# Kernel optimization log

Measured on AMD Instinct MI355X. Metric: run time of the kernel, lower is better.

Reference implementation:

```python
import jax, jax.numpy as jnp
import numpy as np
from jax import lax

EPS = 1e-5
GROUPS = 8
NUM_HEADS = 8


def setup_inputs() -> dict:
    key = jax.random.key(0)
    ks = jax.random.split(key, 3)
    C = 512
    x = jax.random.normal(ks[0], (8, C, 32, 32), dtype=jnp.float32)
    gamma = jnp.ones((C,), jnp.float32)
    beta = jnp.zeros((C,), jnp.float32)
    w_qkv = jax.random.normal(ks[1], (3 * C, C), dtype=jnp.float32) * (1.0 / np.sqrt(C))
    b_qkv = jnp.zeros((3 * C,), jnp.float32)
    w_proj = jax.random.normal(ks[2], (C, C), dtype=jnp.float32) * (1.0 / np.sqrt(C))
    b_proj = jnp.zeros((C,), jnp.float32)
    return {"x": x, "gamma": gamma, "beta": beta, "w_qkv": w_qkv,
            "b_qkv": b_qkv, "w_proj": w_proj, "b_proj": b_proj}


def reference(x, gamma, beta, w_qkv, b_qkv, w_proj, b_proj):
    b, c, h, w = x.shape
    hd = c // NUM_HEADS
    L = h * w
    # GroupNorm over (c/G, h, w) per group
    xg = x.reshape(b, GROUPS, c // GROUPS, h, w)
    mean = jnp.mean(xg, axis=(2, 3, 4), keepdims=True)
    var = jnp.var(xg, axis=(2, 3, 4), keepdims=True)
    xn = ((xg - mean) * lax.rsqrt(var + EPS)).reshape(b, c, h, w)
    xn = xn * gamma[None, :, None, None] + beta[None, :, None, None]
    # 1x1 conv QKV projection over flattened spatial dim
    xr = xn.reshape(b, c, L)
    qkv = jnp.einsum('oc,bcl->bol', w_qkv, xr) + b_qkv[None, :, None]
    q, k, v = jnp.split(qkv, 3, axis=1)
    # [b, H, L, hd]
    q = q.reshape(b, NUM_HEADS, hd, L).transpose(0, 1, 3, 2)
    k = k.reshape(b, NUM_HEADS, hd, L).transpose(0, 1, 3, 2)
    v = v.reshape(b, NUM_HEADS, hd, L).transpose(0, 1, 3, 2)
    scale = 1.0 / np.sqrt(hd).astype(np.float32)
    attn = jnp.einsum('bhqd,bhkd->bhqk', q, k) * scale
    attn = jax.nn.softmax(attn, axis=-1)
    out = jnp.einsum('bhqk,bhkd->bhqd', attn, v)  # [b, H, L, hd]
    out = out.transpose(0, 1, 3, 2).reshape(b, c, L)
    out = jnp.einsum('oc,bcl->bol', w_proj, out) + b_proj[None, :, None]
    return x + out.reshape(b, c, h, w)
```

## Files before the change

kernel.cpp:

```cpp
#include <hip/hip_runtime.h>
#include <hip/hip_bf16.h>

typedef unsigned short u16;
typedef __attribute__((ext_vector_type(8))) short short8;
typedef __attribute__((ext_vector_type(4))) float floatx4;
typedef __attribute__((ext_vector_type(16))) float floatx16;
typedef __attribute__((ext_vector_type(4))) unsigned uint4v;

struct __attribute__((aligned(8))) u16x4 { u16 x, y, z, w; };
struct __attribute__((aligned(16))) u16x8 { u16 v[8]; };

__device__ __forceinline__ u16 f2bf(float f) {
  unsigned u = __builtin_bit_cast(unsigned, f);
  u += 0x7fff + ((u >> 16) & 1);
  return (u16)(u >> 16);
}

__device__ __forceinline__ unsigned cvt_pk_bf16(float lo, float hi) {
  unsigned d;
  asm("v_cvt_pk_bf16_f32 %0, %1, %2" : "=v"(d) : "v"(lo), "v"(hi));
  return d;
}

__device__ __forceinline__ void gload_lds16(const u16* g, u16* l) {
  __builtin_amdgcn_global_load_lds(
      (const __attribute__((address_space(1))) void*)g,
      (__attribute__((address_space(3))) void*)l, 16, 0, 0);
}

__global__ __launch_bounds__(256) void k_convert(
    const float* __restrict__ wq, const float* __restrict__ wp,
    u16* __restrict__ oq, u16* __restrict__ op) {
  int t = blockIdx.x * 256 + threadIdx.x;
  constexpr int NQ4 = (1536 * 512) / 4;
  constexpr int NP4 = (512 * 512) / 4;
  if (t < NQ4) {
    float4 v = reinterpret_cast<const float4*>(wq)[t];
    u16x4 o = { f2bf(v.x), f2bf(v.y), f2bf(v.z), f2bf(v.w) };
    reinterpret_cast<u16x4*>(oq)[t] = o;
  } else if (t - NQ4 < NP4) {
    int i = t - NQ4;
    float4 v = reinterpret_cast<const float4*>(wp)[i];
    u16x4 o = { f2bf(v.x), f2bf(v.y), f2bf(v.z), f2bf(v.w) };
    reinterpret_cast<u16x4*>(op)[i] = o;
  }
}

__global__ __launch_bounds__(256) void k_gn_stats(const float* __restrict__ x,
                                                  float* __restrict__ stats) {
  int bg = blockIdx.x >> 3, sl = blockIdx.x & 7;
  int b = bg >> 3, g = bg & 7;
  const float* base = x + ((size_t)(b * 512 + g * 64) * 1024) + sl * 128;
  float s = 0.f, ss = 0.f;
#pragma unroll
  for (int i = 0; i < 8; ++i) {
    int idx = threadIdx.x + i * 256;
    int c = idx >> 5, l4 = idx & 31;
    float4 v = *reinterpret_cast<const float4*>(base + (size_t)c * 1024 + l4 * 4);
    s += v.x + v.y + v.z + v.w;
    ss += v.x * v.x + v.y * v.y + v.z * v.z + v.w * v.w;
  }
#pragma unroll
  for (int d = 1; d < 64; d <<= 1) { s += __shfl_xor(s, d); ss += __shfl_xor(ss, d); }
  __shared__ float rs[4], rss[4];
  int wid = threadIdx.x >> 6;
  if ((threadIdx.x & 63) == 0) { rs[wid] = s; rss[wid] = ss; }
  __syncthreads();
  if (threadIdx.x == 0) {
    stats[(bg * 8 + sl) * 2]     = rs[0] + rs[1] + rs[2] + rs[3];
    stats[(bg * 8 + sl) * 2 + 1] = rss[0] + rss[1] + rss[2] + rss[3];
  }
}

__global__ __launch_bounds__(256) void k_gn_norm(
    const float* __restrict__ x, const float* __restrict__ gamma,
    const float* __restrict__ beta, const float* __restrict__ stats,
    u16* __restrict__ xnT) {
  int bg = blockIdx.x >> 3, sl = blockIdx.x & 7;
  int b = bg >> 3, g = bg & 7;
  float s = 0.f, ss = 0.f;
#pragma unroll
  for (int i = 0; i < 8; ++i) { s += stats[(bg * 8 + i) * 2]; ss += stats[(bg * 8 + i) * 2 + 1]; }
  const float inv_n = 1.0f / 65536.0f;
  float mean = s * inv_n;
  float var = ss * inv_n - mean * mean;
  float istd = rsqrtf(var + 1e-5f);
  __shared__ float tile[128 * 65];
  const float* base = x + ((size_t)(b * 512 + g * 64) * 1024) + sl * 128;
#pragma unroll
  for (int i = 0; i < 8; ++i) {
    int idx = threadIdx.x + i * 256;
    int c = idx >> 5, l4 = idx & 31;
    float4 v = *reinterpret_cast<const float4*>(base + (size_t)c * 1024 + l4 * 4);
    float gm = gamma[g * 64 + c];
    float ga = gm * istd;
    float be = beta[g * 64 + c] - mean * ga;
    tile[(l4 * 4 + 0) * 65 + c] = v.x * ga + be;
    tile[(l4 * 4 + 1) * 65 + c] = v.y * ga + be;
    tile[(l4 * 4 + 2) * 65 + c] = v.z * ga + be;
    tile[(l4 * 4 + 3) * 65 + c] = v.w * ga + be;
  }
  __syncthreads();
  u16* obase = xnT + ((size_t)(b * 1024 + sl * 128) * 512) + g * 64;
#pragma unroll
  for (int i = 0; i < 8; ++i) {
    int idx = threadIdx.x + i * 256;
    int l = idx >> 4, c4 = (idx & 15) * 4;
    u16x4 o = { f2bf(tile[l * 65 + c4]),     f2bf(tile[l * 65 + c4 + 1]),
                f2bf(tile[l * 65 + c4 + 2]), f2bf(tile[l * 65 + c4 + 3]) };
    *reinterpret_cast<u16x4*>(obase + (size_t)l * 512 + c4) = o;
  }
}

template <int MODE>
__global__ __launch_bounds__(256) void k_gemm(
    const u16* __restrict__ A, const u16* __restrict__ Bm,
    const float* __restrict__ bias, const float* __restrict__ xres,
    u16* __restrict__ Qb, u16* __restrict__ Kb, u16* __restrict__ Vb,
    float* __restrict__ out) {
  int b = blockIdx.x & 7;
  int rem = blockIdx.x >> 3;
  int mt = rem >> 3, nt = rem & 7;
  int tid = threadIdx.x;
  int lane = tid & 63, wid = tid >> 6;
  int wm = wid >> 1, wn = wid & 1;

  union SM {
    u16 ab[2][2][128 * 64];
    u16 c16[128 * 136];
    float c32[128 * 128];
  };
  __shared__ SM sm;

  floatx4 z = {0.f, 0.f, 0.f, 0.f};
  floatx4 acc[4][4];
#pragma unroll
  for (int m = 0; m < 4; ++m)
#pragma unroll
    for (int n = 0; n < 4; ++n) acc[m][n] = z;

  const u16* Abase = A + (size_t)(mt * 128) * 512;
  const u16* Bbase = Bm + ((size_t)(b * 1024 + nt * 128)) * 512;
  int cb0 = (lane & 7) ^ (lane >> 3);
  const u16* asrc = Abase + (size_t)(wid * 32 + (lane >> 3)) * 512 + cb0 * 8;
  const u16* bsrc = Bbase + (size_t)(wid * 32 + (lane >> 3)) * 512 + cb0 * 8;

#define STAGE(BUF, KK)                                                           \
  {                                                                              \
    _Pragma("unroll")                                                            \
    for (int j = 0; j < 4; ++j) {                                                \
      gload_lds16(asrc + (size_t)j * 8 * 512 + (KK) * 64,                        \
                  &sm.ab[BUF][0][wid * 2048 + j * 512]);                         \
      gload_lds16(bsrc + (size_t)j * 8 * 512 + (KK) * 64,                        \
                  &sm.ab[BUF][1][wid * 2048 + j * 512]);                         \
    }                                                                            \
  }

  STAGE(0, 0);
#pragma unroll
  for (int kk = 0; kk < 8; ++kk) {
    const int cur = kk & 1;
    if (kk < 7) {
      STAGE(cur ^ 1, kk + 1);
      asm volatile("s_waitcnt vmcnt(8)" ::: "memory");
    } else {
      asm volatile("s_waitcnt vmcnt(0)" ::: "memory");
    }
    __builtin_amdgcn_s_barrier();
    __builtin_amdgcn_sched_barrier(0);
    const u16* Asc = sm.ab[cur][0];
    const u16* Bsc = sm.ab[cur][1];
#pragma unroll
    for (int kc = 0; kc < 2; ++kc) {
      int cbk = kc * 4 + (lane >> 4);
      short8 af[4], bf[4];
#pragma unroll
      for (int m = 0; m < 4; ++m) {
        int row = wm * 64 + m * 16 + (lane & 15);
        af[m] = *reinterpret_cast<const short8*>(Asc + row * 64 + ((cbk ^ (row & 7)) * 8));
      }
#pragma unroll
      for (int n = 0; n < 4; ++n) {
        int row = wn * 64 + n * 16 + (lane & 15);
        bf[n] = *reinterpret_cast<const short8*>(Bsc + row * 64 + ((cbk ^ (row & 7)) * 8));
      }
#pragma unroll
      for (int m = 0; m < 4; ++m)
#pragma unroll
        for (int n = 0; n < 4; ++n)
          acc[m][n] = __builtin_amdgcn_mfma_f32_16x16x32_bf16(af[m], bf[n], acc[m][n], 0, 0, 0);
    }
    __builtin_amdgcn_s_barrier();
  }
#undef STAGE

  int sec = (MODE == 0) ? (mt >> 2) : 0;
  int ow0 = (mt & 3) * 128;
#pragma unroll
  for (int m = 0; m < 4; ++m) {
#pragma unroll
    for (int n = 0; n < 4; ++n) {
#pragma unroll
      for (int r = 0; r < 4; ++r) {
        int o_l = wm * 64 + m * 16 + ((lane >> 4) * 4) + r;
        int l_l = wn * 64 + n * 16 + (lane & 15);
        float v = acc[m][n][r] + bias[mt * 128 + o_l];
        if (MODE == 0) {
          if (sec == 0) v *= 0.18033688f;
          u16 bv = f2bf(v);
          if (sec < 2) sm.c16[l_l * 136 + o_l] = bv;
          else         sm.c16[o_l * 136 + l_l] = bv;
        } else {
          sm.c32[o_l * 128 + l_l] = v;
        }
      }
    }
  }
  __syncthreads();
  if (MODE == 0) {
    u16* dst = (sec == 0) ? Qb : (sec == 1 ? Kb : Vb);
#pragma unroll
    for (int p = 0; p < 8; ++p) {
      int row = p * 16 + (tid >> 4);
      int col = (tid & 15) * 8;
      u16x8 vv = *reinterpret_cast<const u16x8*>(&sm.c16[row * 136 + col]);
      size_t gi;
      if (sec < 2) gi = ((size_t)(b * 1024 + nt * 128 + row)) * 512 + ow0 + col;
      else         gi = ((size_t)(b * 512 + ow0 + row)) * 1024 + nt * 128 + col;
      *reinterpret_cast<u16x8*>(dst + gi) = vv;
    }
  } else {
#pragma unroll
    for (int p = 0; p < 16; ++p) {
      int row = p * 8 + (tid >> 5);
      int col = (tid & 31) * 4;
      float4 vv = *reinterpret_cast<const float4*>(&sm.c32[row * 128 + col]);
      size_t gi = ((size_t)(b * 512 + mt * 128 + row)) * 1024 + nt * 128 + col;
      float4 xr = *reinterpret_cast<const float4*>(xres + gi);
      vv.x += xr.x; vv.y += xr.y; vv.z += xr.z; vv.w += xr.w;
      *reinterpret_cast<float4*>(out + gi) = vv;
    }
  }
}

__global__ __launch_bounds__(256) void k_attn(
    const u16* __restrict__ Qb, const u16* __restrict__ Kb,
    const u16* __restrict__ Vb, u16* __restrict__ OT) {
  int b = blockIdx.x & 7;
  int h = (blockIdx.x >> 3) & 7;
  int qt = blockIdx.x >> 6;
  int tid = threadIdx.x;
  int lane = tid & 63, wid = tid >> 6;
  int l31 = lane & 31, g = lane >> 5;
  int r7 = l31 & 7;
  __shared__ u16 Ks[64 * 64], Vs[64 * 64];

  short8 qf[4];
  int qrow = qt * 128 + wid * 32 + l31;
  const u16* qp = Qb + ((size_t)(b * 1024 + qrow)) * 512 + h * 64 + g * 8;
#pragma unroll
  for (int kc2 = 0; kc2 < 4; ++kc2)
    qf[kc2] = *reinterpret_cast<const short8*>(qp + kc2 * 16);

  floatx16 oacc[2];
#pragma unroll
  for (int nd = 0; nd < 2; ++nd)
#pragma unroll
    for (int r = 0; r < 16; ++r) oacc[nd][r] = 0.f;
  float m = -1e30f, se = 0.f;

  const u16* ksrc[2]; const u16* vsrc[2]; int sdst[2];
#pragma unroll
  for (int i = 0; i < 2; ++i) {
    int idx = tid + i * 256;
    int row = idx >> 3, cb = idx & 7;
    ksrc[i] = Kb + ((size_t)(b * 1024 + row)) * 512 + h * 64 + cb * 8;
    vsrc[i] = Vb + ((size_t)(b * 512 + h * 64 + row)) * 1024 + cb * 8;
    sdst[i] = row * 64 + ((cb ^ (row & 7)) * 8);
  }
  short8 kreg[2], vreg[2];
#pragma unroll
  for (int i = 0; i < 2; ++i) {
    kreg[i] = *reinterpret_cast<const short8*>(ksrc[i]);
    vreg[i] = *reinterpret_cast<const short8*>(vsrc[i]);
  }

  for (int kt = 0; kt < 16; ++kt) {
#pragma unroll
    for (int i = 0; i < 2; ++i) {
      *reinterpret_cast<short8*>(Ks + sdst[i]) = kreg[i];
      *reinterpret_cast<short8*>(Vs + sdst[i]) = vreg[i];
    }
    __syncthreads();
    if (kt < 15) {
#pragma unroll
      for (int i = 0; i < 2; ++i) {
        kreg[i] = *reinterpret_cast<const short8*>(ksrc[i] + (size_t)(kt + 1) * 64 * 512);
        vreg[i] = *reinterpret_cast<const short8*>(vsrc[i] + (kt + 1) * 64);
      }
    }
    floatx16 sacc[2];
#pragma unroll
    for (int nk = 0; nk < 2; ++nk)
#pragma unroll
      for (int r = 0; r < 16; ++r) sacc[nk][r] = 0.f;
#pragma unroll
    for (int nk = 0; nk < 2; ++nk) {
      const u16* krow = Ks + (nk * 32 + l31) * 64;
#pragma unroll
      for (int kc2 = 0; kc2 < 4; ++kc2) {
        int cb = kc2 * 2 + g;
        short8 kf = *reinterpret_cast<const short8*>(krow + ((cb ^ r7) * 8));
        sacc[nk] = __builtin_amdgcn_mfma_f32_32x32x16_bf16(kf, qf[kc2], sacc[nk], 0, 0, 0);
      }
    }
    float pmax = sacc[0][0];
#pragma unroll
    for (int r = 1; r < 16; ++r) pmax = fmaxf(pmax, sacc[0][r]);
#pragma unroll
    for (int r = 0; r < 16; ++r) pmax = fmaxf(pmax, sacc[1][r]);
    pmax = fmaxf(pmax, __shfl_xor(pmax, 32));
    if (__any(pmax > m + 8.0f)) {
      float mn = fmaxf(m, pmax);
      float f = __builtin_amdgcn_exp2f(m - mn);
      m = mn;
      se *= f;
#pragma unroll
      for (int nd = 0; nd < 2; ++nd)
#pragma unroll
        for (int r = 0; r < 16; ++r) oacc[nd][r] *= f;
    }
    float sum = 0.f;
#pragma unroll
    for (int nk = 0; nk < 2; ++nk)
#pragma unroll
      for (int r = 0; r < 16; ++r) {
        float pv = __builtin_amdgcn_exp2f(sacc[nk][r] - m);
        sacc[nk][r] = pv;
        sum += pv;
      }
    sum += __shfl_xor(sum, 32);
    se += sum;
#pragma unroll
    for (int nk = 0; nk < 2; ++nk) {
#pragma unroll
      for (int kc = 0; kc < 2; ++kc) {
        int base = kc * 8;
        unsigned w0 = cvt_pk_bf16(sacc[nk][base + 0], sacc[nk][base + 1]);
        unsigned w2 = cvt_pk_bf16(sacc[nk][base + 4], sacc[nk][base + 5]);
        auto s0 = __builtin_amdgcn_permlane32_swap((int)w0, (int)w2, false, false);
        unsigned w1 = cvt_pk_bf16(sacc[nk][base + 2], sacc[nk][base + 3]);
        unsigned w3 = cvt_pk_bf16(sacc[nk][base + 6], sacc[nk][base + 7]);
        auto s1 = __builtin_amdgcn_permlane32_swap((int)w1, (int)w3, false, false);
        short8 pf = __builtin_bit_cast(short8,
            uint4v{(unsigned)s0[0], (unsigned)s1[0], (unsigned)s0[1], (unsigned)s1[1]});
#pragma unroll
        for (int nd = 0; nd < 2; ++nd) {
          const u16* vrow = Vs + (nd * 32 + l31) * 64;
          int cb = nk * 4 + kc * 2 + g;
          short8 vf = *reinterpret_cast<const short8*>(vrow + ((cb ^ r7) * 8));
          oacc[nd] = __builtin_amdgcn_mfma_f32_32x32x16_bf16(vf, pf, oacc[nd], 0, 0, 0);
        }
      }
    }
    __syncthreads();
  }
  float inv = 1.0f / se;
  u16* obase = OT + ((size_t)(b * 1024 + qrow)) * 512 + h * 64;
#pragma unroll
  for (int nd = 0; nd < 2; ++nd) {
#pragma unroll
    for (int rq = 0; rq < 4; ++rq) {
      u16x4 o = { f2bf(oacc[nd][rq * 4 + 0] * inv), f2bf(oacc[nd][rq * 4 + 1] * inv),
                  f2bf(oacc[nd][rq * 4 + 2] * inv), f2bf(oacc[nd][rq * 4 + 3] * inv) };
      *reinterpret_cast<u16x4*>(obase + nd * 32 + rq * 8 + g * 4) = o;
    }
  }
}

extern "C" void kernel_launch(void* const* d_in, const int* in_sizes, int n_in,
                              void* d_out, int out_size, void* d_ws, size_t ws_size,
                              hipStream_t stream) {
  const float* x      = (const float*)d_in[0];
  const float* gamma  = (const float*)d_in[1];
  const float* beta   = (const float*)d_in[2];
  const float* w_qkv  = (const float*)d_in[3];
  const float* b_qkv  = (const float*)d_in[4];
  const float* w_proj = (const float*)d_in[5];
  const float* b_proj = (const float*)d_in[6];
  float* out = (float*)d_out;

  char* ws = (char*)d_ws;
  size_t off = 0;
  float* stats = (float*)(ws + off); off += 4096;
  u16* wqb = (u16*)(ws + off); off += (size_t)1536 * 512 * 2;
  u16* wpb = (u16*)(ws + off); off += (size_t)512 * 512 * 2;
  u16* xnT = (u16*)(ws + off); off += (size_t)8 * 1024 * 512 * 2;
  u16* Qb  = (u16*)(ws + off); off += (size_t)8 * 1024 * 512 * 2;
  u16* Kb  = (u16*)(ws + off); off += (size_t)8 * 1024 * 512 * 2;
  u16* Vb  = (u16*)(ws + off); off += (size_t)8 * 1024 * 512 * 2;
  u16* OT  = (u16*)(ws + off); off += (size_t)8 * 1024 * 512 * 2;
  if (ws_size < off) return;

  k_convert<<<1024, 256, 0, stream>>>(w_qkv, w_proj, wqb, wpb);
  k_gn_stats<<<512, 256, 0, stream>>>(x, stats);
  k_gn_norm<<<512, 256, 0, stream>>>(x, gamma, beta, stats, xnT);
  k_gemm<0><<<768, 256, 0, stream>>>(wqb, xnT, b_qkv, nullptr, Qb, Kb, Vb, nullptr);
  k_attn<<<512, 256, 0, stream>>>(Qb, Kb, Vb, OT);
  k_gemm<1><<<256, 256, 0, stream>>>(wpb, OT, b_proj, x, nullptr, nullptr, nullptr, out);
}
```

Measured before the change: 85.98 us.

## Split QKV GEMM into 256x256-tile 8-wave kernel with staged quadrant pipeline

Replaces the templated 128x128 GEMM for the QKV projection with a dedicated kernel that uses 256x256 tiles, 512 threads, and a four-phase schedule. Each phase loads one half of A or B for the next k-step while computing one quadrant of MFMAs. The epilogue is split into two halves so the staging buffer fits in shared memory. Both GEMMs also raise wave priority around their MFMA blocks. Larger tiles increase operand reuse, but with only 192 blocks on 256 CUs part of the GPU sits idle, and the extra barriers add synchronization cost.

```diff
diff --git a/kernel.cpp b/kernel.cpp
--- a/kernel.cpp
+++ b/kernel.cpp
@@ -112,11 +112,188 @@
   }
 }
 
-template <int MODE>
-__global__ __launch_bounds__(256) void k_gemm(
+__global__ __launch_bounds__(512) void k_qkv(
+    const u16* __restrict__ A, const u16* __restrict__ Bm,
+    const float* __restrict__ bias,
+    u16* __restrict__ Qb, u16* __restrict__ Kb, u16* __restrict__ Vb) {
+  int b = blockIdx.x & 7;
+  int rem = blockIdx.x >> 3;
+  int mt = rem >> 2, nt = rem & 3;
+  int tid = threadIdx.x;
+  int lane = tid & 63, wid = tid >> 6;
+  int wm = wid >> 2, wn = wid & 3;
+  int l15 = lane & 15, l4 = lane >> 4;
+
+  union SM {
+    u16 ab[2][2][256 * 64];
+    u16 cqk[256 * 136];
+    u16 cv[128 * 264];
+  };
+  __shared__ SM sm;
+
+  floatx4 acc[8][4];
+#pragma unroll
+  for (int m = 0; m < 8; ++m)
+#pragma unroll
+    for (int n = 0; n < 4; ++n) acc[m][n] = floatx4{0.f, 0.f, 0.f, 0.f};
+
+  const u16* Ab = A + (size_t)(mt * 256) * 512;
+  const u16* Bb = Bm + ((size_t)(b * 1024 + nt * 256)) * 512;
+  int cb0 = (lane & 7) ^ (lane >> 3);
+  const u16* asrc = Ab + (size_t)(wid * 16 + (lane >> 3)) * 512 + cb0 * 8;
+  const u16* bsrc = Bb + (size_t)(wid * 16 + (lane >> 3)) * 512 + cb0 * 8;
+
+  auto STG = [&](int ab, int bufn, int h, int kt) {
+    const u16* s = (ab ? bsrc : asrc) + (size_t)h * 128 * 512 + kt * 64;
+    u16* d = &sm.ab[ab][bufn][(h * 128 + wid * 16) * 64];
+    gload_lds16(s, d);
+    gload_lds16(s + 8 * 512, d + 8 * 64);
+  };
+  auto rd = [&](const u16* base, int rowbase, int kc) -> short8 {
+    int row = rowbase + l15;
+    int cbk = kc * 4 + l4;
+    return *reinterpret_cast<const short8*>(base + row * 64 + ((cbk ^ (row & 7)) * 8));
+  };
+
+  STG(0, 0, 0, 0); STG(1, 0, 0, 0); STG(0, 0, 1, 0); STG(1, 0, 1, 0);
+
+#pragma unroll
+  for (int t = 0; t < 8; ++t) {
+    const int buf = t & 1, nbuf = buf ^ 1;
+    const int kt1 = (t < 7) ? (t + 1) : 7;
+    const u16* Ac = sm.ab[0][buf];
+    const u16* Bc = sm.ab[1][buf];
+    short8 af0[4][2], af1[4][2], bflo[2][2], bfhi[2][2];
+
+    STG(0, nbuf, 0, kt1);
+    asm volatile("s_waitcnt vmcnt(4)" ::: "memory");
+    __builtin_amdgcn_s_barrier();
+    __builtin_amdgcn_sched_barrier(0);
+#pragma unroll
+    for (int m = 0; m < 4; ++m) {
+      af0[m][0] = rd(Ac, m * 32 + wm * 16, 0);
+      af0[m][1] = rd(Ac, m * 32 + wm * 16, 1);
+    }
+#pragma unroll
+    for (int n = 0; n < 2; ++n) {
+      bflo[n][0] = rd(Bc, n * 64 + wn * 16, 0);
+      bflo[n][1] = rd(Bc, n * 64 + wn * 16, 1);
+    }
+    __builtin_amdgcn_s_setprio(1);
+#pragma unroll
+    for (int kc = 0; kc < 2; ++kc)
+#pragma unroll
+      for (int m = 0; m < 4; ++m)
+#pragma unroll
+        for (int n = 0; n < 2; ++n)
+          acc[m][n] = __builtin_amdgcn_mfma_f32_16x16x32_bf16(af0[m][kc], bflo[n][kc], acc[m][n], 0, 0, 0);
+    __builtin_amdgcn_s_setprio(0);
+    __builtin_amdgcn_s_barrier();
+
+    STG(1, nbuf, 0, kt1);
+    asm volatile("s_waitcnt vmcnt(4)" ::: "memory");
+    __builtin_amdgcn_s_barrier();
+    __builtin_amdgcn_sched_barrier(0);
+#pragma unroll
+    for (int m = 0; m < 4; ++m) {
+      af1[m][0] = rd(Ac, 128 + m * 32 + wm * 16, 0);
+      af1[m][1] = rd(Ac, 128 + m * 32 + wm * 16, 1);
+    }
+    __builtin_amdgcn_s_setprio(1);
+#pragma unroll
+    for (int kc = 0; kc < 2; ++kc)
+#pragma unroll
+      for (int m = 0; m < 4; ++m)
+#pragma unroll
+        for (int n = 0; n < 2; ++n)
+          acc[4 + m][n] = __builtin_amdgcn_mfma_f32_16x16x32_bf16(af1[m][kc], bflo[n][kc], acc[4 + m][n], 0, 0, 0);
+    __builtin_amdgcn_s_setprio(0);
+    __builtin_amdgcn_s_barrier();
+
+    STG(0, nbuf, 1, kt1);
+    __builtin_amdgcn_s_barrier();
+#pragma unroll
+    for (int n = 0; n < 2; ++n) {
+      bfhi[n][0] = rd(Bc, 128 + n * 64 + wn * 16, 0);
+      bfhi[n][1] = rd(Bc, 128 + n * 64 + wn * 16, 1);
+    }
+    __builtin_amdgcn_s_setprio(1);
+#pragma unroll
+    for (int kc = 0; kc < 2; ++kc)
+#pragma unroll
+      for (int m = 0; m < 4; ++m)
+#pragma unroll
+        for (int n = 0; n < 2; ++n)
+          acc[4 + m][2 + n] = __builtin_amdgcn_mfma_f32_16x16x32_bf16(af1[m][kc], bfhi[n][kc], acc[4 + m][2 + n], 0, 0, 0);
+    __builtin_amdgcn_s_setprio(0);
+    __builtin_amdgcn_s_barrier();
+
+    STG(1, nbuf, 1, kt1);
+    __builtin_amdgcn_s_barrier();
+    __builtin_amdgcn_s_setprio(1);
+#pragma unroll
+    for (int kc = 0; kc < 2; ++kc)
+#pragma unroll
+      for (int m = 0; m < 4; ++m)
+#pragma unroll
+        for (int n = 0; n < 2; ++n)
+          acc[m][2 + n] = __builtin_amdgcn_mfma_f32_16x16x32_bf16(af0[m][kc], bfhi[n][kc], acc[m][2 + n], 0, 0, 0);
+    __builtin_amdgcn_s_setprio(0);
+    __builtin_amdgcn_s_barrier();
+  }
+
+  asm volatile("s_waitcnt vmcnt(0)" ::: "memory");
+  __syncthreads();
+  int sec = mt >> 1;
+  int osec = (mt & 1) * 256;
+  const float* bs = bias + mt * 256;
+  float scale = (sec == 0) ? 0.18033688f : 1.0f;
+  u16* dst = (sec == 0) ? Qb : (sec == 1 ? Kb : Vb);
+#pragma unroll
+  for (int half = 0; half < 2; ++half) {
+#pragma unroll
+    for (int mm = 0; mm < 4; ++mm) {
+      int m = half * 4 + mm;
+#pragma unroll
+      for (int n = 0; n < 4; ++n) {
+#pragma unroll
+        for (int r = 0; r < 4; ++r) {
+          int o_l = m * 32 + wm * 16 + l4 * 4 + r;
+          int l_l = n * 64 + wn * 16 + l15;
+          float v = (acc[m][n][r] + bs[o_l]) * scale;
+          int oh = o_l - half * 128;
+          if (sec < 2) sm.cqk[l_l * 136 + oh] = f2bf(v);
+          else         sm.cv[oh * 264 + l_l] = f2bf(v);
+        }
+      }
+    }
+    __syncthreads();
+    if (sec < 2) {
+#pragma unroll
+      for (int p = 0; p < 8; ++p) {
+        int row = p * 32 + (tid >> 4);
+        int col = (tid & 15) * 8;
+        u16x8 vv = *reinterpret_cast<const u16x8*>(&sm.cqk[row * 136 + col]);
+        size_t gi = ((size_t)(b * 1024 + nt * 256 + row)) * 512 + osec + half * 128 + col;
+        *reinterpret_cast<u16x8*>(dst + gi) = vv;
+      }
+    } else {
+#pragma unroll
+      for (int p = 0; p < 8; ++p) {
+        int row = p * 16 + (tid >> 5);
+        int col = (tid & 31) * 8;
+        u16x8 vv = *reinterpret_cast<const u16x8*>(&sm.cv[row * 264 + col]);
+        size_t gi = ((size_t)(b * 512 + osec + half * 128 + row)) * 1024 + nt * 256 + col;
+        *reinterpret_cast<u16x8*>(dst + gi) = vv;
+      }
+    }
+    __syncthreads();
+  }
+}
+
+__global__ __launch_bounds__(256) void k_proj(
     const u16* __restrict__ A, const u16* __restrict__ Bm,
     const float* __restrict__ bias, const float* __restrict__ xres,
-    u16* __restrict__ Qb, u16* __restrict__ Kb, u16* __restrict__ Vb,
     float* __restrict__ out) {
   int b = blockIdx.x & 7;
   int rem = blockIdx.x >> 3;
@@ -127,17 +304,15 @@
 
   union SM {
     u16 ab[2][2][128 * 64];
-    u16 c16[128 * 136];
     float c32[128 * 128];
   };
   __shared__ SM sm;
 
-  floatx4 z = {0.f, 0.f, 0.f, 0.f};
   floatx4 acc[4][4];
 #pragma unroll
   for (int m = 0; m < 4; ++m)
 #pragma unroll
-    for (int n = 0; n < 4; ++n) acc[m][n] = z;
+    for (int n = 0; n < 4; ++n) acc[m][n] = floatx4{0.f, 0.f, 0.f, 0.f};
 
   const u16* Abase = A + (size_t)(mt * 128) * 512;
   const u16* Bbase = Bm + ((size_t)(b * 1024 + nt * 128)) * 512;
@@ -145,31 +320,31 @@
   const u16* asrc = Abase + (size_t)(wid * 32 + (lane >> 3)) * 512 + cb0 * 8;
   const u16* bsrc = Bbase + (size_t)(wid * 32 + (lane >> 3)) * 512 + cb0 * 8;
 
-#define STAGE(BUF, KK)                                                           \
+#define PSTAGE(BUF, KK)                                                          \
   {                                                                              \
     _Pragma("unroll")                                                            \
     for (int j = 0; j < 4; ++j) {                                                \
       gload_lds16(asrc + (size_t)j * 8 * 512 + (KK) * 64,                        \
-                  &sm.ab[BUF][0][wid * 2048 + j * 512]);                         \
+                  &sm.ab[0][BUF][(wid * 32 + j * 8) * 64]);                      \
       gload_lds16(bsrc + (size_t)j * 8 * 512 + (KK) * 64,                        \
-                  &sm.ab[BUF][1][wid * 2048 + j * 512]);                         \
+                  &sm.ab[1][BUF][(wid * 32 + j * 8) * 64]);                      \
     }                                                                            \
   }
 
-  STAGE(0, 0);
+  PSTAGE(0, 0);
 #pragma unroll
   for (int kk = 0; kk < 8; ++kk) {
     const int cur = kk & 1;
     if (kk < 7) {
-      STAGE(cur ^ 1, kk + 1);
+      PSTAGE(cur ^ 1, kk + 1);
       asm volatile("s_waitcnt vmcnt(8)" ::: "memory");
     } else {
       asm volatile("s_waitcnt vmcnt(0)" ::: "memory");
     }
     __builtin_amdgcn_s_barrier();
     __builtin_amdgcn_sched_barrier(0);
-    const u16* Asc = sm.ab[cur][0];
-    const u16* Bsc = sm.ab[cur][1];
+    const u16* Asc = sm.ab[0][cur];
+    const u16* Bsc = sm.ab[1][cur];
 #pragma unroll
     for (int kc = 0; kc < 2; ++kc) {
       int cbk = kc * 4 + (lane >> 4);
@@ -184,62 +359,38 @@
         int row = wn * 64 + n * 16 + (lane & 15);
         bf[n] = *reinterpret_cast<const short8*>(Bsc + row * 64 + ((cbk ^ (row & 7)) * 8));
       }
+      __builtin_amdgcn_s_setprio(1);
 #pragma unroll
       for (int m = 0; m < 4; ++m)
 #pragma unroll
         for (int n = 0; n < 4; ++n)
           acc[m][n] = __builtin_amdgcn_mfma_f32_16x16x32_bf16(af[m], bf[n], acc[m][n], 0, 0, 0);
-    }
-    __builtin_amdgcn_s_barrier();
-  }
-#undef STAGE
-
-  int sec = (MODE == 0) ? (mt >> 2) : 0;
-  int ow0 = (mt & 3) * 128;
-#pragma unroll
-  for (int m = 0; m < 4; ++m) {
-#pragma unroll
-    for (int n = 0; n < 4; ++n) {
+      __builtin_amdgcn_s_setprio(0);
+    }
+    __builtin_amdgcn_s_barrier();
+  }
+#undef PSTAGE
+
+#pragma unroll
+  for (int m = 0; m < 4; ++m)
+#pragma unroll
+    for (int n = 0; n < 4; ++n)
 #pragma unroll
       for (int r = 0; r < 4; ++r) {
         int o_l = wm * 64 + m * 16 + ((lane >> 4) * 4) + r;
         int l_l = wn * 64 + n * 16 + (lane & 15);
-        float v = acc[m][n][r] + bias[mt * 128 + o_l];
-        if (MODE == 0) {
-          if (sec == 0) v *= 0.18033688f;
-          u16 bv = f2bf(v);
-          if (sec < 2) sm.c16[l_l * 136 + o_l] = bv;
-          else         sm.c16[o_l * 136 + l_l] = bv;
-        } else {
-          sm.c32[o_l * 128 + l_l] = v;
-        }
-      }
-    }
-  }
+        sm.c32[o_l * 128 + l_l] = acc[m][n][r] + bias[mt * 128 + o_l];
+      }
   __syncthreads();
-  if (MODE == 0) {
-    u16* dst = (sec == 0) ? Qb : (sec == 1 ? Kb : Vb);
-#pragma unroll
-    for (int p = 0; p < 8; ++p) {
-      int row = p * 16 + (tid >> 4);
-      int col = (tid & 15) * 8;
-      u16x8 vv = *reinterpret_cast<const u16x8*>(&sm.c16[row * 136 + col]);
-      size_t gi;
-      if (sec < 2) gi = ((size_t)(b * 1024 + nt * 128 + row)) * 512 + ow0 + col;
-      else         gi = ((size_t)(b * 512 + ow0 + row)) * 1024 + nt * 128 + col;
-      *reinterpret_cast<u16x8*>(dst + gi) = vv;
-    }
-  } else {
-#pragma unroll
-    for (int p = 0; p < 16; ++p) {
-      int row = p * 8 + (tid >> 5);
-      int col = (tid & 31) * 4;
-      float4 vv = *reinterpret_cast<const float4*>(&sm.c32[row * 128 + col]);
-      size_t gi = ((size_t)(b * 512 + mt * 128 + row)) * 1024 + nt * 128 + col;
-      float4 xr = *reinterpret_cast<const float4*>(xres + gi);
-      vv.x += xr.x; vv.y += xr.y; vv.z += xr.z; vv.w += xr.w;
-      *reinterpret_cast<float4*>(out + gi) = vv;
-    }
+#pragma unroll
+  for (int p = 0; p < 16; ++p) {
+    int row = p * 8 + (tid >> 5);
+    int col = (tid & 31) * 4;
+    float4 vv = *reinterpret_cast<const float4*>(&sm.c32[row * 128 + col]);
+    size_t gi = ((size_t)(b * 512 + mt * 128 + row)) * 1024 + nt * 128 + col;
+    float4 xr = *reinterpret_cast<const float4*>(xres + gi);
+    vv.x += xr.x; vv.y += xr.y; vv.z += xr.z; vv.w += xr.w;
+    *reinterpret_cast<float4*>(out + gi) = vv;
   }
 }
 
@@ -405,7 +556,7 @@
   k_convert<<<1024, 256, 0, stream>>>(w_qkv, w_proj, wqb, wpb);
   k_gn_stats<<<512, 256, 0, stream>>>(x, stats);
   k_gn_norm<<<512, 256, 0, stream>>>(x, gamma, beta, stats, xnT);
-  k_gemm<0><<<768, 256, 0, stream>>>(wqb, xnT, b_qkv, nullptr, Qb, Kb, Vb, nullptr);
+  k_qkv<<<192, 512, 0, stream>>>(wqb, xnT, b_qkv, Qb, Kb, Vb);
   k_attn<<<512, 256, 0, stream>>>(Qb, Kb, Vb, OT);
-  k_gemm<1><<<256, 256, 0, stream>>>(wpb, OT, b_proj, x, nullptr, nullptr, nullptr, out);
-}
+  k_proj<<<256, 256, 0, stream>>>(wpb, OT, b_proj, x, out);
+}
```

Measured after the change: 86.86 us. No clear change (+1.0%).
